# Kernel tuning notes

Measured on AMD Instinct MI355X. Metric: run time of the kernel, lower is better.

The kernel has to match this reference:

```python
import jax, jax.numpy as jnp
import numpy as np

N_GRAPHS = 512  # number of graphs in the batch
S2S_STEPS = 3   # Set2Set processing_steps


def segment_softmax(e, seg, num_seg):
    m = jax.ops.segment_max(e, seg, num_segments=num_seg)
    ex = jnp.exp(e - m[seg])
    s = jax.ops.segment_sum(ex, seg, num_segments=num_seg)
    return ex / s[seg]


def setup_inputs() -> dict:
    key = jax.random.key(0)
    ks = jax.random.split(key, 24)
    N, E, Fin, Fe, D = 30000, 480000, 25, 14, 256
    s = 0.05
    inp = {
        "x": jax.random.normal(ks[0], (N, Fin), jnp.float32),
        "edge_attr": jax.random.normal(ks[1], (E, Fe), jnp.float32),
        # lin0
        "W0": jax.random.normal(ks[2], (Fin, D), jnp.float32) * s,
        "b0": jnp.zeros((D,), jnp.float32),
        # DMPNN edge-message MLP: [x_src || e_attr] -> D -> D
        "Wm1": jax.random.normal(ks[3], (D + Fe, D), jnp.float32) * s,
        "bm1": jnp.zeros((D,), jnp.float32),
        "Wm2": jax.random.normal(ks[4], (D, D), jnp.float32) * s,
        "bm2": jnp.zeros((D,), jnp.float32),
        # node (root) update
        "Wr": jax.random.normal(ks[5], (D, D), jnp.float32) * s,
        "br": jnp.zeros((D,), jnp.float32),
        # Set2Set LSTM: input 2D -> hidden D
        "Wih": jax.random.normal(ks[6], (2 * D, 4 * D), jnp.float32) * s,
        "Whh": jax.random.normal(ks[7], (D, 4 * D), jnp.float32) * s,
        "bl": jnp.zeros((4 * D,), jnp.float32),
        # readout MLP
        "W1": jax.random.normal(ks[8], (2 * D, D), jnp.float32) * s,
        "b1": jnp.zeros((D,), jnp.float32),
        "W2": jax.random.normal(ks[9], (D, 1), jnp.float32) * s,
        "b2": jnp.zeros((1,), jnp.float32),
        "edge_index": jax.random.randint(ks[10], (2, E), 0, N, jnp.int32),
        "batch": jnp.sort(jax.random.randint(ks[11], (N,), 0, N_GRAPHS, jnp.int32)),
    }
    return inp


def reference(x, edge_attr, W0, b0, Wm1, bm1, Wm2, bm2, Wr, br,
              Wih, Whh, bl, W1, b1, W2, b2, edge_index, batch):
    N = x.shape[0]
    # lin0 + relu
    h0 = jax.nn.relu(x @ W0 + b0)  # [N, D]
    # DMPNNLayer2: edge-conditioned message, sum-aggregate, root update (eval: no dropout)
    src, dst = edge_index[0], edge_index[1]
    m = jax.nn.relu(jnp.concatenate([h0[src], edge_attr], axis=-1) @ Wm1 + bm1)  # [E, D]
    m = m @ Wm2 + bm2
    agg = jax.ops.segment_sum(m, dst, num_segments=N)  # [N, D]
    out = jax.nn.relu(h0 @ Wr + br + agg)  # relu in top-level forward, massage_depth=1
    # Set2Set pooling (processing_steps=3)
    D = out.shape[1]
    B = N_GRAPHS
    q_star = jnp.zeros((B, 2 * D), out.dtype)
    h = jnp.zeros((B, D), out.dtype)
    c = jnp.zeros((B, D), out.dtype)
    for _ in range(S2S_STEPS):
        gates = q_star @ Wih + h @ Whh + bl  # [B, 4D]
        i, f, g, o = jnp.split(gates, 4, axis=-1)
        c = jax.nn.sigmoid(f) * c + jax.nn.sigmoid(i) * jnp.tanh(g)
        h = jax.nn.sigmoid(o) * jnp.tanh(c)
        e = jnp.sum(out * h[batch], axis=-1)              # [N]
        a = segment_softmax(e, batch, B)                  # [N]
        r = jax.ops.segment_sum(a[:, None] * out, batch, num_segments=B)  # [B, D]
        q_star = jnp.concatenate([h, r], axis=-1)
    # readout (eval: dropout identity)
    y = jax.nn.relu(q_star @ W1 + b1)
    y = y @ W2 + b2
    return y.reshape(-1)
```

## Files before the change

### kernel.cpp

```cpp
#include <hip/hip_runtime.h>

typedef unsigned short u16;
typedef unsigned char u8;
typedef unsigned int u32;
using s16x8 = __attribute__((ext_vector_type(8))) short;
using s16x4 = __attribute__((ext_vector_type(4))) short;
using f32x4 = __attribute__((ext_vector_type(4))) float;

#define DEV static __device__ __forceinline__

DEV float b2f(u16 u) { return __uint_as_float(((u32)u) << 16); }
DEV u16 f2bu(float f) {
    u32 u = __float_as_uint(f);
    u32 r = (u + 0x7FFFu + ((u >> 16) & 1u)) >> 16;
    return (u16)r;
}
DEV float sigm(float x) { return 1.0f / (1.0f + expf(-x)); }

DEV float ldv(const void* p, int i, int f32flag) {
    if (f32flag) return ((const float*)p)[i];
    return b2f(((const u16*)p)[i]);
}
DEV void stv(void* p, int i, float v, int f32flag) {
    if (f32flag) ((float*)p)[i] = v;
    else ((u16*)p)[i] = f2bu(v);
}

DEV int lower_bound(const int* b, int n, int v) {
    int lo = 0, hi = n;
    while (lo < hi) { int mid = (lo + hi) >> 1; if (b[mid] < v) lo = mid + 1; else hi = mid; }
    return lo;
}

__global__ void DMPNN_Change_678604832935_kernel(int* p) {
    if (p && threadIdx.x == 0 && blockIdx.x == 0) p[0] = 1;
}

__global__ void detect_kernel(const void* x, int* flag) {
    __shared__ int cnt[128];
    int tid = threadIdx.x;
    if (tid < 128) {
        u16 v = ((const u16*)x)[tid];
        int e = (v >> 7) & 0xFF;
        cnt[tid] = (e >= 100 && e <= 141) ? 1 : 0;
    }
    __syncthreads();
    if (tid == 0) {
        int s = 0;
        for (int i = 0; i < 128; ++i) s += cnt[i];
        flag[0] = (s < 110) ? 1 : 0;
    }
}

__global__ void init_kernel(const void* x, int* flag, void* out, int* stub) {
    __shared__ int cnt[128];
    __shared__ int fsh;
    int tid = threadIdx.x;
    if (tid < 128) {
        u16 v = ((const u16*)x)[tid];
        int e = (v >> 7) & 0xFF;
        cnt[tid] = (e >= 100 && e <= 141) ? 1 : 0;
    }
    __syncthreads();
    if (tid == 0) {
        int s = 0;
        for (int i = 0; i < 128; ++i) s += cnt[i];
        int f = (s < 110) ? 1 : 0;
        flag[0] = f;
        fsh = f;
        if (stub) stub[0] = 1;
    }
    __syncthreads();
    int f32 = fsh;
    for (int i = tid; i < 512; i += 256) stv(out, i, 3.0f, f32);
}

__global__ void fillv_kernel(void* out, const int* flag, float v) {
    int i = blockIdx.x * 256 + threadIdx.x;
    if (i < 512) stv(out, i, v, flag[0]);
}

__global__ void zero_kernel(float* p, int n) {
    int i = blockIdx.x * 256 + threadIdx.x;
    int stride = gridDim.x * 256;
    for (; i < n; i += stride) p[i] = 0.0f;
}

__global__ void zero2_kernel(float* a, int na, float* b, int nb) {
    int i = blockIdx.x * 256 + threadIdx.x;
    int stride = gridDim.x * 256;
    for (int j = i; j < na; j += stride) a[j] = 0.0f;
    for (int j = i; j < nb; j += stride) b[j] = 0.0f;
}

__global__ void hist_kernel(const int* __restrict__ eidx, u32* __restrict__ cnt) {
    int i = blockIdx.x * 256 + threadIdx.x;
    if (i < 480000) atomicAdd(&cnt[eidx[480000 + i]], 1u);
}

__global__ void scan1_kernel(const u32* __restrict__ cnt, u32* __restrict__ part) {
    __shared__ u32 s[256];
    int i = blockIdx.x * 256 + threadIdx.x;
    s[threadIdx.x] = (i < 30000) ? cnt[i] : 0u;
    __syncthreads();
    for (int st = 128; st > 0; st >>= 1) {
        if (threadIdx.x < st) s[threadIdx.x] += s[threadIdx.x + st];
        __syncthreads();
    }
    if (threadIdx.x == 0) part[blockIdx.x] = s[0];
}

__global__ void scan3_kernel(u32* __restrict__ cursor, const u32* __restrict__ part) {
    __shared__ u32 s[256];
    __shared__ u32 pbase;
    int b = blockIdx.x, tid = threadIdx.x;
    {
        u32 v = (tid < 118 && tid < b) ? part[tid] : 0u;
        s[tid] = v;
        __syncthreads();
        for (int st = 128; st > 0; st >>= 1) {
            if (tid < st) s[tid] += s[tid + st];
            __syncthreads();
        }
        if (tid == 0) pbase = s[0];
        __syncthreads();
    }
    int i = b * 256 + tid;
    u32 v = (i < 30000) ? cursor[i] : 0u;
    s[tid] = v;
    __syncthreads();
    for (int off = 1; off < 256; off <<= 1) {
        u32 t = (tid >= off) ? s[tid - off] : 0u;
        __syncthreads();
        s[tid] += t;
        __syncthreads();
    }
    u32 excl = s[tid] - v + pbase;
    if (i < 30000) cursor[i] = excl;
}

__global__ void scatter_kernel(const int* __restrict__ eidx, u32* __restrict__ cursor,
                               u16* __restrict__ permLo, u8* __restrict__ permHi,
                               u16* __restrict__ srcW) {
    int i = blockIdx.x * 256 + threadIdx.x;
    if (i < 480000) {
        int d = eidx[480000 + i];
        u32 pos = atomicAdd(&cursor[d], 1u);
        permLo[pos] = (u16)(i & 0xFFFF);
        permHi[pos] = (u8)(i >> 16);
        if (srcW) srcW[pos] = (u16)eidx[i];
    }
}

__global__ void to_blocked_all(const void* Wm1, const void* Wm2, const void* Wr,
                               const void* Wih, const void* Whh,
                               const void* eattr, const int* flag,
                               u16* Wm1b, u16* Wm2b, u16* Wrb, u16* Wcatb,
                               u16* eattrB) {
    const int T1 = 9 * 4 * 256 * 8;
    const int T2 = T1 + 8 * 4 * 256 * 8;
    const int T3 = T2 + 8 * 4 * 256 * 8;
    const int T4 = T3 + 24 * 4 * 1024 * 8;
    const int T5 = T4 + 480000 * 14;
    int idx = blockIdx.x * 256 + threadIdx.x;
    int f32 = flag[0];
    if (idx >= T4) {
        if (eattrB && idx < T5) {
            int l = idx - T4;
            eattrB[l] = f2bu(ldv(eattr, l, f32));
        }
        return;
    }
    if (idx < T3) {
        const void* src; u16* dst; int K; int l;
        if (idx < T1)      { src = Wm1; dst = Wm1b; K = 270; l = idx; }
        else if (idx < T2) { src = Wm2; dst = Wm2b; K = 256; l = idx - T1; }
        else               { src = Wr;  dst = Wrb;  K = 256; l = idx - T2; }
        int c = l & 7;
        int n = (l >> 3) & 255;
        int jk = l >> 11;
        int j = jk & 3, kt = jk >> 2;
        int k = kt * 32 + j * 8 + c;
        u16 v = 0;
        if (k < K) v = f2bu(ldv(src, k * 256 + n, f32));
        dst[l] = v;
    } else {
        int l = idx - T3;
        int c = l & 7;
        int n = (l >> 3) & 1023;
        int jk = l >> 13;
        int j = jk & 3, kt = jk >> 2;
        int k = kt * 32 + j * 8 + c;
        u16 v = 0;
        if (k < 512) v = f2bu(ldv(Wih, k * 1024 + n, f32));
        else if (k < 768) v = f2bu(ldv(Whh, (k - 512) * 1024 + n, f32));
        Wcatb[l] = v;
    }
}

__global__ __launch_bounds__(256) void lin0_kernel(const void* x, const void* W0,
                                                   const void* b0, const int* flag,
                                                   u16* h0b) {
    int f32 = flag[0];
    int n0 = blockIdx.x * 8, tid = threadIdx.x;
    __shared__ float xs[8][26];
    if (tid < 200) {
        int nn = tid / 25, k = tid % 25;
        xs[nn][k] = ldv(x, (n0 + nn) * 25 + k, f32);
    }
    __syncthreads();
    float wr[25];
    #pragma unroll
    for (int k = 0; k < 25; ++k) wr[k] = ldv(W0, k * 256 + tid, f32);
    float bias = ldv(b0, tid, f32);
    #pragma unroll
    for (int nn = 0; nn < 8; ++nn) {
        float a = bias;
        #pragma unroll
        for (int k = 0; k < 25; ++k) a += xs[nn][k] * wr[k];
        h0b[(n0 + nn) * 256 + tid] = f2bu(fmaxf(a, 0.0f));
    }
}

__global__ __launch_bounds__(256) void lin0q_kernel(
    const void* x, const void* W0, const void* b0, const int* flag,
    const u16* __restrict__ Wm1b, u16* __restrict__ h0b, u16* __restrict__ Qb) {
    __shared__ __attribute__((aligned(16))) u16 As[64 * 264];
    __shared__ float xs[64][26];
    const int f32 = flag[0];
    const int tid = threadIdx.x;
    const int w = tid >> 6, lane = tid & 63, quad = lane >> 4, mrow = lane & 15;
    const int row0 = blockIdx.x * 64;
    const int colb = w * 64 + mrow;

    for (int idx = tid; idx < 64 * 25; idx += 256) {
        int i = idx / 25, k = idx - i * 25;
        int row = row0 + i;
        xs[i][k] = (row < 30000) ? ldv(x, row * 25 + k, f32) : 0.0f;
    }
    float wr[25];
    #pragma unroll
    for (int k = 0; k < 25; ++k) wr[k] = ldv(W0, k * 256 + tid, f32);
    float bias = ldv(b0, tid, f32);
    __syncthreads();
    for (int i = 0; i < 64; ++i) {
        float a = bias;
        #pragma unroll
        for (int k = 0; k < 25; ++k) a += xs[i][k] * wr[k];
        u16 hb = f2bu(fmaxf(a, 0.0f));
        As[i * 264 + tid] = hb;
        int row = row0 + i;
        if (row < 30000) h0b[row * 256 + tid] = hb;
    }
    __syncthreads();

    f32x4 acc[4][4];
    f32x4 fzero = {0.f, 0.f, 0.f, 0.f};
    #pragma unroll
    for (int mi = 0; mi < 4; ++mi)
        #pragma unroll
        for (int ni = 0; ni < 4; ++ni) acc[mi][ni] = fzero;

    for (int kt = 0; kt < 8; ++kt) {
        s16x8 af[4], bf[4];
        #pragma unroll
        for (int ni = 0; ni < 4; ++ni)
            bf[ni] = *(const s16x8*)(Wm1b + (((kt * 4 + quad) * 256) + colb + ni * 16) * 8);
        #pragma unroll
        for (int mi = 0; mi < 4; ++mi)
            af[mi] = *(const s16x8*)(As + (mi * 16 + mrow) * 264 + kt * 32 + quad * 8);
        #pragma unroll
        for (int mi = 0; mi < 4; ++mi)
            #pragma unroll
            for (int ni = 0; ni < 4; ++ni)
                acc[mi][ni] = __builtin_amdgcn_mfma_f32_16x16x32_bf16(af[mi], bf[ni], acc[mi][ni], 0, 0, 0);
    }

    #pragma unroll
    for (int mi = 0; mi < 4; ++mi)
        #pragma unroll
        for (int rg = 0; rg < 4; ++rg) {
            int row = row0 + mi * 16 + quad * 4 + rg;
            if (row >= 30000) continue;
            #pragma unroll
            for (int ni = 0; ni < 4; ++ni)
                Qb[row * 256 + colb + ni * 16] = f2bu(acc[mi][ni][rg]);
        }
}

__global__ __launch_bounds__(256) void qgen_kernel(
    const u16* __restrict__ h0b, const u16* __restrict__ Wm1b,
    u16* __restrict__ Qb) {
    __shared__ __attribute__((aligned(16))) u16 As[64 * 264];
    const int tid = threadIdx.x;
    const int w = tid >> 6, lane = tid & 63, quad = lane >> 4, mrow = lane & 15;
    const int row0 = blockIdx.x * 64;
    const int colb = w * 64 + mrow;
    const int r = tid >> 2, sub = tid & 3;

    {
        int row = row0 + r;
        u16* arow = As + r * 264;
        #pragma unroll
        for (int j = 0; j < 8; ++j) {
            int c0 = sub * 64 + j * 8;
            s16x8 v = {0, 0, 0, 0, 0, 0, 0, 0};
            if (row < 30000) v = *(const s16x8*)(h0b + row * 256 + c0);
            *(s16x8*)(arow + c0) = v;
        }
    }
    __syncthreads();

    f32x4 acc[4][4];
    f32x4 fzero = {0.f, 0.f, 0.f, 0.f};
    #pragma unroll
    for (int mi = 0; mi < 4; ++mi)
        #pragma unroll
        for (int ni = 0; ni < 4; ++ni) acc[mi][ni] = fzero;

    for (int kt = 0; kt < 8; ++kt) {
        s16x8 af[4], bf[4];
        #pragma unroll
        for (int ni = 0; ni < 4; ++ni)
            bf[ni] = *(const s16x8*)(Wm1b + (((kt * 4 + quad) * 256) + colb + ni * 16) * 8);
        #pragma unroll
        for (int mi = 0; mi < 4; ++mi)
            af[mi] = *(const s16x8*)(As + (mi * 16 + mrow) * 264 + kt * 32 + quad * 8);
        #pragma unroll
        for (int mi = 0; mi < 4; ++mi)
            #pragma unroll
            for (int ni = 0; ni < 4; ++ni)
                acc[mi][ni] = __builtin_amdgcn_mfma_f32_16x16x32_bf16(af[mi], bf[ni], acc[mi][ni], 0, 0, 0);
    }

    #pragma unroll
    for (int mi = 0; mi < 4; ++mi)
        #pragma unroll
        for (int rg = 0; rg < 4; ++rg) {
            int row = row0 + mi * 16 + quad * 4 + rg;
            if (row >= 30000) continue;
            #pragma unroll
            for (int ni = 0; ni < 4; ++ni)
                Qb[row * 256 + colb + ni * 16] = f2bu(acc[mi][ni][rg]);
        }
}

#define MAXD 96
__global__ __launch_bounds__(256) void edge_mfma_node2_kernel(
    const u16* __restrict__ Qb, const void* __restrict__ eattr,
    const u16* __restrict__ eattrB,
    const u16* __restrict__ srcW,
    const u16* __restrict__ permLo, const u8* __restrict__ permHi,
    const u32* __restrict__ cursor,
    const u16* __restrict__ Wm1b, const void* __restrict__ bm1,
    const int* __restrict__ flag, u16* __restrict__ aggB) {
    const int f32 = flag[0];
    const int n = blockIdx.x, tid = threadIdx.x;
    const int w = tid >> 6, lane = tid & 63, quad = lane >> 4, mrow = lane & 15;
    const int beg = (n > 0) ? (int)cursor[n - 1] : 0;
    const int end = (int)cursor[n];
    __shared__ int eids[MAXD];
    __shared__ int srcl[MAXD];
    __shared__ int sorted_s[MAXD];
    __shared__ int sortedSrc[MAXD];
    __shared__ __attribute__((aligned(16))) u16 Ae[16 * 40];

    const int colb = w * 64 + mrow;
    s16x8 bf[4];
    float bm1c[4];
    #pragma unroll
    for (int ni = 0; ni < 4; ++ni) {
        bf[ni] = *(const s16x8*)(Wm1b + (((32 + quad) * 256) + colb + ni * 16) * 8);
        bm1c[ni] = ldv(bm1, colb + ni * 16, f32);
    }

    float psum[4] = {0.f, 0.f, 0.f, 0.f};
    const f32x4 fzero = {0.f, 0.f, 0.f, 0.f};

    for (int base = beg; base < end; base += MAXD) {
        int wcnt = end - base; if (wcnt > MAXD) wcnt = MAXD;
        if (tid < wcnt) {
            int si = base + tid;
            eids[tid] = (int)permLo[si] | ((int)permHi[si] << 16);
            srcl[tid] = (int)srcW[si];
        }
        __syncthreads();
        if (tid < wcnt) {
            int key = eids[tid], r2 = 0;
            for (int j = 0; j < wcnt; ++j) r2 += (eids[j] < key);
            sorted_s[r2] = key;
            sortedSrc[r2] = srcl[tid];
        }
        __syncthreads();

        for (int cb = 0; cb < wcnt; cb += 16) {
            {
                int row = tid >> 4, c = tid & 15;
                int gi = cb + row;
                int e = (gi < wcnt) ? sorted_s[gi] : -1;
                u16 v = 0;
                if (e >= 0 && c < 14)
                    v = eattrB ? eattrB[e * 14 + c] : f2bu(ldv(eattr, e * 14 + c, f32));
                Ae[row * 40 + c] = v;
                Ae[row * 40 + 16 + c] = 0;
            }
            __syncthreads();

            float qv[4][4];
            #pragma unroll
            for (int rg = 0; rg < 4; ++rg) {
                int gi = cb + quad * 4 + rg;
                int sidx = (gi < wcnt) ? sortedSrc[gi] : 0;
                const u16* qrow = Qb + sidx * 256;
                #pragma unroll
                for (int ni = 0; ni < 4; ++ni)
                    qv[rg][ni] = b2f(qrow[colb + ni * 16]);
            }

            s16x8 af = *(const s16x8*)(Ae + mrow * 40 + quad * 8);
            f32x4 acc[4];
            #pragma unroll
            for (int ni = 0; ni < 4; ++ni)
                acc[ni] = __builtin_amdgcn_mfma_f32_16x16x32_bf16(af, bf[ni], fzero, 0, 0, 0);

            #pragma unroll
            for (int rg = 0; rg < 4; ++rg) {
                if (cb + quad * 4 + rg < wcnt) {
                    #pragma unroll
                    for (int ni = 0; ni < 4; ++ni)
                        psum[ni] += fmaxf(acc[ni][rg] + bm1c[ni] + qv[rg][ni], 0.0f);
                }
            }
            __syncthreads();
        }
    }

    #pragma unroll
    for (int ni = 0; ni < 4; ++ni) {
        float v = psum[ni];
        v += __shfl_xor(v, 16, 64);
        v += __shfl_xor(v, 32, 64);
        psum[ni] = v;
    }
    if (quad == 0) {
        #pragma unroll
        for (int ni = 0; ni < 4; ++ni)
            aggB[n * 256 + colb + ni * 16] = f2bu(psum[ni]);
    }
}

__global__ __launch_bounds__(256) void edge_mfma_node_kernel(
    const u16* __restrict__ Qb, const void* __restrict__ eattr,
    const int* __restrict__ eidx,
    const u16* __restrict__ permLo, const u8* __restrict__ permHi,
    const u32* __restrict__ cursor,
    const u16* __restrict__ Wm1b, const void* __restrict__ bm1,
    const int* __restrict__ flag, float* __restrict__ aggP) {
    const int f32 = flag[0];
    const int n = blockIdx.x, tid = threadIdx.x;
    const int w = tid >> 6, lane = tid & 63, quad = lane >> 4, mrow = lane & 15;
    const int beg = (n > 0) ? (int)cursor[n - 1] : 0;
    const int end = (int)cursor[n];
    __shared__ int eids[MAXD];
    __shared__ int sorted_s[MAXD];
    __shared__ int srcs16[16];
    __shared__ __attribute__((aligned(16))) u16 Ae[16 * 40];

    const int colb = w * 64 + mrow;
    s16x8 bf[4];
    float bm1c[4];
    #pragma unroll
    for (int ni = 0; ni < 4; ++ni) {
        bf[ni] = *(const s16x8*)(Wm1b + (((32 + quad) * 256) + colb + ni * 16) * 8);
        bm1c[ni] = ldv(bm1, colb + ni * 16, f32);
    }

    float psum[4] = {0.f, 0.f, 0.f, 0.f};
    const f32x4 fzero = {0.f, 0.f, 0.f, 0.f};

    for (int base = beg; base < end; base += MAXD) {
        int wcnt = end - base; if (wcnt > MAXD) wcnt = MAXD;
        if (tid < wcnt) {
            int si = base + tid;
            eids[tid] = (int)permLo[si] | ((int)permHi[si] << 16);
        }
        __syncthreads();
        if (tid < wcnt) {
            int key = eids[tid], r2 = 0;
            for (int j = 0; j < wcnt; ++j) r2 += (eids[j] < key);
            sorted_s[r2] = key;
        }
        __syncthreads();

        for (int cb = 0; cb < wcnt; cb += 16) {
            {
                int row = tid >> 4, c = tid & 15;
                int gi = cb + row;
                int e = (gi < wcnt) ? sorted_s[gi] : -1;
                u16 v = 0;
                if (e >= 0 && c < 14) v = f2bu(ldv(eattr, e * 14 + c, f32));
                Ae[row * 40 + c] = v;
                Ae[row * 40 + 16 + c] = 0;
                if (c == 0) srcs16[row] = (e >= 0) ? eidx[e] : 0;
            }
            __syncthreads();

            s16x8 af = *(const s16x8*)(Ae + mrow * 40 + quad * 8);
            f32x4 acc[4];
            #pragma unroll
            for (int ni = 0; ni < 4; ++ni)
                acc[ni] = __builtin_amdgcn_mfma_f32_16x16x32_bf16(af, bf[ni], fzero, 0, 0, 0);

            #pragma unroll
            for (int rg = 0; rg < 4; ++rg) {
                int row = quad * 4 + rg;
                if (cb + row < wcnt) {
                    const u16* qrow = Qb + srcs16[row] * 256;
                    #pragma unroll
                    for (int ni = 0; ni < 4; ++ni) {
                        float q = b2f(qrow[colb + ni * 16]);
                        psum[ni] += fmaxf(acc[ni][rg] + bm1c[ni] + q, 0.0f);
                    }
                }
            }
            __syncthreads();
        }
    }

    #pragma unroll
    for (int ni = 0; ni < 4; ++ni) {
        float v = psum[ni];
        v += __shfl_xor(v, 16, 64);
        v += __shfl_xor(v, 32, 64);
        psum[ni] = v;
    }
    if (quad == 0) {
        #pragma unroll
        for (int ni = 0; ni < 4; ++ni)
            aggP[n * 256 + colb + ni * 16] = psum[ni];
    }
}

__global__ __launch_bounds__(256) void edge_sorted_kernel(
    const u16* __restrict__ h0b, const void* __restrict__ eattr,
    const int* __restrict__ eidx,
    const u16* __restrict__ permLo, const u8* __restrict__ permHi,
    const u16* __restrict__ Wm1b,
    const void* __restrict__ bm1,
    const int* __restrict__ flag, float* __restrict__ aggP) {
    __shared__ __attribute__((aligned(16))) u16 As[64 * 296];
    __shared__ int dsh[64];
    const int f32 = flag[0];
    const int tid = threadIdx.x;
    const int w = tid >> 6, lane = tid & 63, quad = lane >> 4, mrow = lane & 15;
    const int eb0 = blockIdx.x * 64;
    const int colb = w * 64 + mrow;

    if (tid < 64) {
        int sj = eb0 + tid;
        int ee = (int)permLo[sj] | ((int)permHi[sj] << 16);
        dsh[tid] = eidx[480000 + ee];
    }
    {
        int r = tid >> 2, sub = tid & 3;
        int si = eb0 + r;
        int e = (int)permLo[si] | ((int)permHi[si] << 16);
        int src = eidx[e];
        const u16* hrow = h0b + src * 256;
        u16* arow = As + r * 296;
        #pragma unroll
        for (int j = 0; j < 8; ++j) {
            int c0 = sub * 64 + j * 8;
            *(s16x8*)(arow + c0) = *(const s16x8*)(hrow + c0);
        }
        if (sub == 0) {
            for (int c = 0; c < 14; ++c) arow[256 + c] = f2bu(ldv(eattr, e * 14 + c, f32));
            for (int c = 14; c < 40; ++c) arow[256 + c] = 0;
        }
    }
    __syncthreads();

    f32x4 acc[4][4];
    f32x4 fzero = {0.f, 0.f, 0.f, 0.f};
    #pragma unroll
    for (int mi = 0; mi < 4; ++mi)
        #pragma unroll
        for (int ni = 0; ni < 4; ++ni) acc[mi][ni] = fzero;

    for (int kt = 0; kt < 9; ++kt) {
        s16x8 af[4], bf[4];
        #pragma unroll
        for (int ni = 0; ni < 4; ++ni)
            bf[ni] = *(const s16x8*)(Wm1b + (((kt * 4 + quad) * 256) + colb + ni * 16) * 8);
        #pragma unroll
        for (int mi = 0; mi < 4; ++mi)
            af[mi] = *(const s16x8*)(As + (mi * 16 + mrow) * 296 + kt * 32 + quad * 8);
        #pragma unroll
        for (int mi = 0; mi < 4; ++mi)
            #pragma unroll
            for (int ni = 0; ni < 4; ++ni)
                acc[mi][ni] = __builtin_amdgcn_mfma_f32_16x16x32_bf16(af[mi], bf[ni], acc[mi][ni], 0, 0, 0);
    }

    float bm1c[4];
    #pragma unroll
    for (int ni = 0; ni < 4; ++ni) bm1c[ni] = ldv(bm1, colb + ni * 16, f32);
    __syncthreads();
    #pragma unroll
    for (int mi = 0; mi < 4; ++mi)
        #pragma unroll
        for (int ni = 0; ni < 4; ++ni)
            #pragma unroll
            for (int rg = 0; rg < 4; ++rg) {
                int row = mi * 16 + quad * 4 + rg;
                As[row * 296 + colb + ni * 16] = f2bu(fmaxf(acc[mi][ni][rg] + bm1c[ni], 0.0f));
            }
    __syncthreads();

    {
        int c = tid;
        float s = 0.0f;
        int cur = dsh[0];
        #pragma unroll 8
        for (int rr = 0; rr < 64; ++rr) {
            int d = dsh[rr];
            if (d != cur) { atomicAdd(&aggP[cur * 256 + c], s); s = 0.0f; cur = d; }
            s += b2f(As[rr * 296 + c]);
        }
        atomicAdd(&aggP[cur * 256 + c], s);
    }
}

__global__ __launch_bounds__(256) void node_dual_kernel(
    u16* __restrict__ h0b, const u16* __restrict__ Wrb, const u16* __restrict__ Wm2b,
    const void* __restrict__ br, const void* __restrict__ bm2,
    const void* __restrict__ aggV, int agg_bf16,
    const u32* __restrict__ cursor,
    const int* __restrict__ flag) {
    __shared__ __attribute__((aligned(16))) u16 As[64 * 264];
    const int f32 = flag[0];
    const int tid = threadIdx.x;
    const int w = tid >> 6, lane = tid & 63, quad = lane >> 4, mrow = lane & 15;
    const int row0 = blockIdx.x * 64;
    const int colb = w * 64 + mrow;
    const int r = tid >> 2, sub = tid & 3;

    {
        int row = row0 + r;
        u16* arow = As + r * 264;
        #pragma unroll
        for (int j = 0; j < 8; ++j) {
            int c0 = sub * 64 + j * 8;
            s16x8 v = {0, 0, 0, 0, 0, 0, 0, 0};
            if (row < 30000) v = *(const s16x8*)(h0b + row * 256 + c0);
            *(s16x8*)(arow + c0) = v;
        }
    }
    __syncthreads();

    f32x4 acc[4][4];
    f32x4 fzero = {0.f, 0.f, 0.f, 0.f};
    #pragma unroll
    for (int mi = 0; mi < 4; ++mi)
        #pragma unroll
        for (int ni = 0; ni < 4; ++ni) acc[mi][ni] = fzero;

    for (int kt = 0; kt < 8; ++kt) {
        s16x8 af[4], bf[4];
        #pragma unroll
        for (int ni = 0; ni < 4; ++ni)
            bf[ni] = *(const s16x8*)(Wrb + (((kt * 4 + quad) * 256) + colb + ni * 16) * 8);
        #pragma unroll
        for (int mi = 0; mi < 4; ++mi)
            af[mi] = *(const s16x8*)(As + (mi * 16 + mrow) * 264 + kt * 32 + quad * 8);
        #pragma unroll
        for (int mi = 0; mi < 4; ++mi)
            #pragma unroll
            for (int ni = 0; ni < 4; ++ni)
                acc[mi][ni] = __builtin_amdgcn_mfma_f32_16x16x32_bf16(af[mi], bf[ni], acc[mi][ni], 0, 0, 0);
    }
    __syncthreads();

    {
        int row = row0 + r;
        u16* arow = As + r * 264;
        if (agg_bf16) {
            const u16* aggB = (const u16*)aggV;
            #pragma unroll
            for (int j = 0; j < 8; ++j) {
                int c0 = sub * 64 + j * 8;
                s16x8 v = {0, 0, 0, 0, 0, 0, 0, 0};
                if (row < 30000) v = *(const s16x8*)(aggB + row * 256 + c0);
                *(s16x8*)(arow + c0) = v;
            }
        } else {
            const float* aggP = (const float*)aggV;
            #pragma unroll
            for (int j = 0; j < 8; ++j) {
                int c0 = sub * 64 + j * 8;
                s16x8 pk = {0, 0, 0, 0, 0, 0, 0, 0};
                if (row < 30000) {
                    f32x4 a = *(const f32x4*)(aggP + row * 256 + c0);
                    f32x4 b = *(const f32x4*)(aggP + row * 256 + c0 + 4);
                    pk[0] = (short)f2bu(a[0]); pk[1] = (short)f2bu(a[1]);
                    pk[2] = (short)f2bu(a[2]); pk[3] = (short)f2bu(a[3]);
                    pk[4] = (short)f2bu(b[0]); pk[5] = (short)f2bu(b[1]);
                    pk[6] = (short)f2bu(b[2]); pk[7] = (short)f2bu(b[3]);
                }
                *(s16x8*)(arow + c0) = pk;
            }
        }
    }
    __syncthreads();

    for (int kt = 0; kt < 8; ++kt) {
        s16x8 af[4], bf[4];
        #pragma unroll
        for (int ni = 0; ni < 4; ++ni)
            bf[ni] = *(const s16x8*)(Wm2b + (((kt * 4 + quad) * 256) + colb + ni * 16) * 8);
        #pragma unroll
        for (int mi = 0; mi < 4; ++mi)
            af[mi] = *(const s16x8*)(As + (mi * 16 + mrow) * 264 + kt * 32 + quad * 8);
        #pragma unroll
        for (int mi = 0; mi < 4; ++mi)
            #pragma unroll
            for (int ni = 0; ni < 4; ++ni)
                acc[mi][ni] = __builtin_amdgcn_mfma_f32_16x16x32_bf16(af[mi], bf[ni], acc[mi][ni], 0, 0, 0);
    }

    #pragma unroll
    for (int mi = 0; mi < 4; ++mi)
        #pragma unroll
        for (int rg = 0; rg < 4; ++rg) {
            int row = row0 + mi * 16 + quad * 4 + rg;
            if (row >= 30000) continue;
            float dg = (float)(cursor[row] - (row > 0 ? cursor[row - 1] : 0u));
            #pragma unroll
            for (int ni = 0; ni < 4; ++ni) {
                int col = colb + ni * 16;
                float v = acc[mi][ni][rg] + ldv(br, col, f32) + dg * ldv(bm2, col, f32);
                h0b[row * 256 + col] = f2bu(fmaxf(v, 0.0f));
            }
        }
}

__global__ __launch_bounds__(256) void gates_mfma_kernel(
    const u16* __restrict__ Abuf, const u16* __restrict__ Wcatb,
    float* __restrict__ G) {
    const int tid = threadIdx.x;
    const int w = tid >> 6, lane = tid & 63, quad = lane >> 4, mrow = lane & 15;
    const int row0 = blockIdx.x * 64;
    const int col = blockIdx.y * 64 + w * 16 + mrow;

    f32x4 acc[4];
    f32x4 fzero = {0.f, 0.f, 0.f, 0.f};
    #pragma unroll
    for (int mi = 0; mi < 4; ++mi) acc[mi] = fzero;

    for (int kt = 0; kt < 24; ++kt) {
        s16x8 bfv = *(const s16x8*)(Wcatb + (((kt * 4 + quad) * 1024) + col) * 8);
        s16x8 af[4];
        #pragma unroll
        for (int mi = 0; mi < 4; ++mi)
            af[mi] = *(const s16x8*)(Abuf + (row0 + mi * 16 + mrow) * 768 + kt * 32 + quad * 8);
        #pragma unroll
        for (int mi = 0; mi < 4; ++mi)
            acc[mi] = __builtin_amdgcn_mfma_f32_16x16x32_bf16(af[mi], bfv, acc[mi], 0, 0, 0);
    }

    #pragma unroll
    for (int mi = 0; mi < 4; ++mi)
        #pragma unroll
        for (int rg = 0; rg < 4; ++rg)
            G[(row0 + mi * 16 + quad * 4 + rg) * 1024 + col] = acc[mi][rg];
}

#define GROWS 112
__global__ __launch_bounds__(256) void s2s_lstm_fused_kernel(
    const float* __restrict__ G, const void* __restrict__ bl,
    const int* __restrict__ flag, float* __restrict__ Cst, float* __restrict__ Hst,
    const u16* __restrict__ outb, const int* __restrict__ batch,
    float* __restrict__ Rst, u16* __restrict__ Abuf, float* __restrict__ ebuf) {
    __shared__ __attribute__((aligned(16))) u16 Ls[GROWS * 256];
    __shared__ __attribute__((aligned(16))) float hsh[256];
    __shared__ float esh[GROWS];
    __shared__ float red[256];
    const int b = blockIdx.x, tid = threadIdx.x;
    const int w = tid >> 6, lane = tid & 63;
    const int f32 = flag[0];

    {
        float gi = G[b * 1024 + tid]       + ldv(bl, tid, f32);
        float gf = G[b * 1024 + 256 + tid] + ldv(bl, 256 + tid, f32);
        float gg = G[b * 1024 + 512 + tid] + ldv(bl, 512 + tid, f32);
        float go = G[b * 1024 + 768 + tid] + ldv(bl, 768 + tid, f32);
        float c = Cst[b * 256 + tid];
        c = sigm(gf) * c + sigm(gi) * tanhf(gg);
        Cst[b * 256 + tid] = c;
        float h = sigm(go) * tanhf(c);
        Hst[b * 256 + tid] = h;
        u16 hb = f2bu(h);
        Abuf[b * 768 + tid] = hb;
        Abuf[b * 768 + 512 + tid] = hb;
        hsh[tid] = h;
    }
    const int n0 = lower_bound(batch, 30000, b);
    const int n1 = lower_bound(batch, 30000, b + 1);
    const int cnt = n1 - n0;
    __syncthreads();
    float r_out = 0.0f;
    if (cnt > 0 && cnt <= GROWS) {
        for (int idx = tid; idx < cnt * 32; idx += 256) {
            int i = idx >> 5, c8 = idx & 31;
            *(s16x8*)(Ls + i * 256 + c8 * 8) = *(const s16x8*)(outb + (n0 + i) * 256 + c8 * 8);
        }
        __syncthreads();
        for (int i = w; i < cnt; i += 4) {
            s16x4 ov = *(const s16x4*)(Ls + i * 256 + lane * 4);
            f32x4 hv = *(const f32x4*)(hsh + lane * 4);
            float p = b2f((u16)ov[0]) * hv[0] + b2f((u16)ov[1]) * hv[1]
                    + b2f((u16)ov[2]) * hv[2] + b2f((u16)ov[3]) * hv[3];
            #pragma unroll
            for (int off = 1; off < 64; off <<= 1) p += __shfl_xor(p, off, 64);
            if (lane == 0) esh[i] = p;
        }
        __syncthreads();
        float m = -1e30f;
        for (int i = tid; i < cnt; i += 256) m = fmaxf(m, esh[i]);
        red[tid] = m; __syncthreads();
        for (int s = 128; s > 0; s >>= 1) { if (tid < s) red[tid] = fmaxf(red[tid], red[tid + s]); __syncthreads(); }
        m = red[0]; __syncthreads();
        float sl = 0.0f;
        for (int i = tid; i < cnt; i += 256) { float pe = expf(esh[i] - m); esh[i] = pe; sl += pe; }
        red[tid] = sl; __syncthreads();
        for (int s = 128; s > 0; s >>= 1) { if (tid < s) red[tid] += red[tid + s]; __syncthreads(); }
        float ssum = red[0]; __syncthreads();
        float acc = 0.0f;
        for (int i = 0; i < cnt; ++i) acc += esh[i] * b2f(Ls[i * 256 + tid]);
        r_out = acc / ssum;
    } else if (cnt > GROWS) {
        for (int i = w; i < cnt; i += 4) {
            const u16* orow = outb + (n0 + i) * 256 + lane * 4;
            f32x4 hv = *(const f32x4*)(hsh + lane * 4);
            float p = b2f(orow[0]) * hv[0] + b2f(orow[1]) * hv[1]
                    + b2f(orow[2]) * hv[2] + b2f(orow[3]) * hv[3];
            #pragma unroll
            for (int off = 1; off < 64; off <<= 1) p += __shfl_xor(p, off, 64);
            if (lane == 0) ebuf[n0 + i] = p;
        }
        __syncthreads();
        float m = -1e30f;
        for (int n = n0 + tid; n < n1; n += 256) m = fmaxf(m, ebuf[n]);
        red[tid] = m; __syncthreads();
        for (int s = 128; s > 0; s >>= 1) { if (tid < s) red[tid] = fmaxf(red[tid], red[tid + s]); __syncthreads(); }
        m = red[0]; __syncthreads();
        float sl = 0.0f;
        for (int n = n0 + tid; n < n1; n += 256) sl += expf(ebuf[n] - m);
        red[tid] = sl; __syncthreads();
        for (int s = 128; s > 0; s >>= 1) { if (tid < s) red[tid] += red[tid + s]; __syncthreads(); }
        float ssum = red[0]; __syncthreads();
        float acc = 0.0f;
        for (int c0 = n0; c0 < n1; c0 += 256) {
            int nn = n1 - c0; if (nn > 256) nn = 256;
            __syncthreads();
            if (tid < nn) red[tid] = expf(ebuf[c0 + tid] - m);
            __syncthreads();
            for (int i = 0; i < nn; ++i) acc += red[i] * b2f(outb[(c0 + i) * 256 + tid]);
        }
        r_out = acc / ssum;
    }
    Rst[b * 256 + tid] = r_out;
    Abuf[b * 768 + 256 + tid] = f2bu(r_out);
}

__global__ __launch_bounds__(256) void readout_kernel(const float* Hst, const float* Rst,
                                                      const void* W1, const void* b1,
                                                      const void* W2, const void* b2,
                                                      const u16* nodeout, const void* aggV,
                                                      int agg_bf16,
                                                      const int* flag, void* out) {
    int f32 = flag[0];
    int b = blockIdx.x, tid = threadIdx.x;
    __shared__ float qs[512];
    __shared__ float red[256];
    qs[tid] = Hst[b * 256 + tid];
    qs[256 + tid] = Rst[b * 256 + tid];
    __syncthreads();
    float a = ldv(b1, tid, f32);
    if (f32) {
        const float* W1f = (const float*)W1;
        #pragma unroll 8
        for (int k = 0; k < 512; ++k) a += qs[k] * W1f[k * 256 + tid];
    } else {
        const u16* W1h = (const u16*)W1;
        #pragma unroll 8
        for (int k = 0; k < 512; ++k) a += qs[k] * b2f(W1h[k * 256 + tid]);
    }
    a = fmaxf(a, 0.0f) * ldv(W2, tid, f32);
    red[tid] = a; __syncthreads();
    for (int s = 128; s > 0; s >>= 1) { if (tid < s) red[tid] += red[tid + s]; __syncthreads(); }
    if (tid == 0) {
        float D = 0.0f;
        if (b == 0) {
            float s1 = 0.0f, s2 = 0.0f, s3 = 0.0f;
            for (int i = 0; i < 256; ++i) {
                s1 += fabsf(b2f(nodeout[i]));
                s2 += agg_bf16 ? fabsf(b2f(((const u16*)aggV)[i]))
                               : fabsf(((const float*)aggV)[i]);
                s3 += fabsf(Rst[i]);
            }
            if (s1 < 1e-3f) D += 100.0f;
            if (s2 < 1e-3f) D += 200.0f;
            if (s3 < 1e-6f) D += 400.0f;
        }
        stv(out, b, red[0] + ldv(b2, 0, f32) + D, f32);
    }
}

#define OFF_FLAG 0
#define OFF_HST  64
#define OFF_RST  524352
#define OFF_CST  1048640
#define OFF_PLO  64
#define OFF_PHI  960064
#define OFF_CUR  1440064
#define OFF_WREG 1572928
#define OFF_WM1B (OFF_WREG)
#define OFF_WM2B (OFF_WREG + 147456)
#define OFF_WRB  (OFF_WREG + 278528)
#define OFF_WCAT (OFF_WREG + 409600)
#define OFF_E    3670080
#define OFF_AGG  3790144
#define OFF_ABUF (OFF_AGG + 1048576)
#define OFF_G    (OFF_AGG + 4194304)
#define OFF_H0B  34510144
#define WS_NEEDED 49870144
#define OFF_Q    49870144
#define WS_FAST  (49870144 + 15360000)
#define OFF_SRC  (OFF_Q + 15360000)
#define WS_FAST2 (OFF_SRC + 960000)
#define OFF_EATB (OFF_SRC + 960000)
#define WS_FAST3 (OFF_EATB + 13440000)

extern "C" __attribute__((visibility("default")))
void kernel_launch(void* const* d_in, const int* in_sizes, int n_in,
                   void* d_out, int out_size, void* d_ws, size_t ws_size,
                   hipStream_t stream) {
    char* ws = (char*)d_ws;
    int*   flag   = (int*)(ws + OFF_FLAG);
    float* Hst    = (float*)(ws + OFF_HST);
    float* Rst    = (float*)(ws + OFF_RST);
    float* Cst    = (float*)(ws + OFF_CST);
    u16*   permLo = (u16*)(ws + OFF_PLO);
    u8*    permHi = (u8*)(ws + OFF_PHI);
    u32*   cursor = (u32*)(ws + OFF_CUR);
    u16*   Wm1b   = (u16*)(ws + OFF_WM1B);
    u16*   Wm2b   = (u16*)(ws + OFF_WM2B);
    u16*   Wrb    = (u16*)(ws + OFF_WRB);
    u16*   Wcatb  = (u16*)(ws + OFF_WCAT);
    float* ebuf   = (float*)(ws + OFF_E);
    u32*   part   = (u32*)(ws + OFF_E);
    float* aggP   = (float*)(ws + OFF_AGG);
    u16*   Abuf   = (u16*)(ws + OFF_ABUF);
    float* G      = (float*)(ws + OFF_G);
    u16*   h0b    = (u16*)(ws + OFF_H0B);
    u16*   Qb     = (u16*)(ws + OFF_Q);
    u16*   srcW   = (u16*)(ws + OFF_SRC);
    u16*   eattrB = (u16*)(ws + OFF_EATB);

    bool sizes_ok = (n_in == 19)
        && in_sizes[0] == 30000 * 25
        && in_sizes[1] == 480000 * 14
        && in_sizes[4] == 270 * 256
        && in_sizes[10] == 512 * 1024
        && in_sizes[17] == 2 * 480000
        && in_sizes[18] == 30000;
    if (!sizes_ok) {
        detect_kernel<<<1, 256, 0, stream>>>(d_in[0], flag);
        fillv_kernel<<<2, 256, 0, stream>>>(d_out, flag, 1600.0f);
        return;
    }
    if (ws_size < (size_t)WS_NEEDED) {
        detect_kernel<<<1, 256, 0, stream>>>(d_in[0], flag);
        fillv_kernel<<<2, 256, 0, stream>>>(d_out, flag, 800.0f);
        return;
    }
    const int fastlvl = (ws_size >= (size_t)WS_FAST3) ? 3
                      : (ws_size >= (size_t)WS_FAST2) ? 2
                      : (ws_size >= (size_t)WS_FAST)  ? 1 : 0;

    const void* x     = d_in[0];
    const void* eattr = d_in[1];
    const void* W0    = d_in[2];
    const void* b0    = d_in[3];
    const void* Wm1   = d_in[4];
    const void* bm1   = d_in[5];
    const void* Wm2   = d_in[6];
    const void* bm2   = d_in[7];
    const void* Wr    = d_in[8];
    const void* br    = d_in[9];
    const void* Wih   = d_in[10];
    const void* Whh   = d_in[11];
    const void* bl    = d_in[12];
    const void* W1    = d_in[13];
    const void* b1    = d_in[14];
    const void* W2    = d_in[15];
    const void* b2    = d_in[16];
    const int* eidx   = (const int*)d_in[17];
    const int* batch  = (const int*)d_in[18];

    init_kernel<<<1, 256, 0, stream>>>(x, flag, d_out, (int*)(ws + OFF_G));

    {
        int total = (fastlvl >= 3) ? (991232 + 480000 * 14) : 991232;
        int grid = (total + 255) / 256;
        to_blocked_all<<<grid, 256, 0, stream>>>(Wm1, Wm2, Wr, Wih, Whh, eattr, flag,
                                                 Wm1b, Wm2b, Wrb, Wcatb,
                                                 (fastlvl >= 3) ? eattrB : (u16*)nullptr);
    }

    if (fastlvl >= 1) {
        lin0q_kernel<<<469, 256, 0, stream>>>(x, W0, b0, flag, Wm1b, h0b, Qb);
    } else {
        lin0_kernel<<<3750, 256, 0, stream>>>(x, W0, b0, flag, h0b);
    }

    zero_kernel<<<30, 256, 0, stream>>>((float*)cursor, 30000);
    hist_kernel<<<1875, 256, 0, stream>>>(eidx, cursor);
    scan1_kernel<<<118, 256, 0, stream>>>(cursor, part);
    scan3_kernel<<<118, 256, 0, stream>>>(cursor, part);
    scatter_kernel<<<1875, 256, 0, stream>>>(eidx, cursor, permLo, permHi,
                                             (fastlvl >= 2) ? srcW : (u16*)nullptr);

    int agg_bf16 = 0;
    if (fastlvl >= 2) {
        agg_bf16 = 1;
        edge_mfma_node2_kernel<<<30000, 256, 0, stream>>>(
            Qb, eattr, (fastlvl >= 3) ? eattrB : (u16*)nullptr,
            srcW, permLo, permHi, cursor, Wm1b, bm1, flag, (u16*)aggP);
    } else if (fastlvl == 1) {
        edge_mfma_node_kernel<<<30000, 256, 0, stream>>>(Qb, eattr, eidx, permLo, permHi,
                                                         cursor, Wm1b, bm1, flag, aggP);
    } else {
        zero_kernel<<<1024, 256, 0, stream>>>(aggP, 7680000);
        edge_sorted_kernel<<<7500, 256, 0, stream>>>(h0b, eattr, eidx, permLo, permHi,
                                                     Wm1b, bm1, flag, aggP);
    }
    node_dual_kernel<<<469, 256, 0, stream>>>(h0b, Wrb, Wm2b, br, bm2,
                                              aggP, agg_bf16, cursor, flag);

    zero2_kernel<<<256, 256, 0, stream>>>(Cst, 131072, (float*)Abuf, 196608);

    for (int s = 0; s < 3; ++s) {
        gates_mfma_kernel<<<dim3(8, 16), 256, 0, stream>>>(Abuf, Wcatb, G);
        s2s_lstm_fused_kernel<<<512, 256, 0, stream>>>(G, bl, flag, Cst, Hst,
                                                       h0b, batch, Rst, Abuf, ebuf);
    }
    readout_kernel<<<512, 256, 0, stream>>>(Hst, Rst, W1, b1, W2, b2, h0b,
                                            aggP, agg_bf16, flag, d_out);
}
```

Baseline: 460.0 us.

## Pre-permute edge attributes by destination and add simplified per-node edge kernel

During the scatter pass, the bf16 edge attributes are copied into destination-sorted order in a new workspace buffer. A new per-node edge kernel then reads those attributes contiguously together with the sorted source indices, with no permutation lookups and no per-node sorting or staging of edge ids. This is meant to cut gather indirection and shared-memory bookkeeping in the edge stage. In exchange it needs extra workspace and a scattered 14-element copy per edge in the scatter kernel, and it only runs when the workspace is large enough.

```diff
diff --git a/kernel.cpp b/kernel.cpp
--- a/kernel.cpp
+++ b/kernel.cpp
@@ -141,7 +141,8 @@
 
 __global__ void scatter_kernel(const int* __restrict__ eidx, u32* __restrict__ cursor,
                                u16* __restrict__ permLo, u8* __restrict__ permHi,
-                               u16* __restrict__ srcW) {
+                               u16* __restrict__ srcW,
+                               const u16* __restrict__ eattrB, u16* __restrict__ eattrS) {
     int i = blockIdx.x * 256 + threadIdx.x;
     if (i < 480000) {
         int d = eidx[480000 + i];
@@ -149,6 +150,10 @@
         permLo[pos] = (u16)(i & 0xFFFF);
         permHi[pos] = (u8)(i >> 16);
         if (srcW) srcW[pos] = (u16)eidx[i];
+        if (eattrS) {
+            #pragma unroll
+            for (int c = 0; c < 14; ++c) eattrS[pos * 14 + c] = eattrB[i * 14 + c];
+        }
     }
 }
 
@@ -346,6 +351,85 @@
 }
 
 #define MAXD 96
+__global__ __launch_bounds__(256) void edge_mfma_node3_kernel(
+    const u16* __restrict__ Qb, const u16* __restrict__ eattrS,
+    const u16* __restrict__ srcW,
+    const u32* __restrict__ cursor,
+    const u16* __restrict__ Wm1b, const void* __restrict__ bm1,
+    const int* __restrict__ flag, u16* __restrict__ aggB) {
+    const int f32 = flag[0];
+    const int n = blockIdx.x, tid = threadIdx.x;
+    const int w = tid >> 6, lane = tid & 63, quad = lane >> 4, mrow = lane & 15;
+    const int beg = (n > 0) ? (int)cursor[n - 1] : 0;
+    const int end = (int)cursor[n];
+    __shared__ int srcs16[16];
+    __shared__ __attribute__((aligned(16))) u16 Ae[16 * 40];
+
+    const int colb = w * 64 + mrow;
+    s16x8 bf[4];
+    float bm1c[4];
+    #pragma unroll
+    for (int ni = 0; ni < 4; ++ni) {
+        bf[ni] = *(const s16x8*)(Wm1b + (((32 + quad) * 256) + colb + ni * 16) * 8);
+        bm1c[ni] = ldv(bm1, colb + ni * 16, f32);
+    }
+
+    float psum[4] = {0.f, 0.f, 0.f, 0.f};
+    const f32x4 fzero = {0.f, 0.f, 0.f, 0.f};
+
+    for (int cb = beg; cb < end; cb += 16) {
+        int m = end - cb; if (m > 16) m = 16;
+        {
+            int row = tid >> 4, c = tid & 15;
+            u16 v = 0;
+            if (row < m && c < 14) v = eattrS[(cb + row) * 14 + c];
+            Ae[row * 40 + c] = v;
+            Ae[row * 40 + 16 + c] = 0;
+            if (c == 0) srcs16[row] = (row < m) ? (int)srcW[cb + row] : 0;
+        }
+        __syncthreads();
+
+        float qv[4][4];
+        #pragma unroll
+        for (int rg = 0; rg < 4; ++rg) {
+            int sidx = srcs16[quad * 4 + rg];
+            const u16* qrow = Qb + sidx * 256;
+            #pragma unroll
+            for (int ni = 0; ni < 4; ++ni)
+                qv[rg][ni] = b2f(qrow[colb + ni * 16]);
+        }
+
+        s16x8 af = *(const s16x8*)(Ae + mrow * 40 + quad * 8);
+        f32x4 acc[4];
+        #pragma unroll
+        for (int ni = 0; ni < 4; ++ni)
+            acc[ni] = __builtin_amdgcn_mfma_f32_16x16x32_bf16(af, bf[ni], fzero, 0, 0, 0);
+
+        #pragma unroll
+        for (int rg = 0; rg < 4; ++rg) {
+            if (quad * 4 + rg < m) {
+                #pragma unroll
+                for (int ni = 0; ni < 4; ++ni)
+                    psum[ni] += fmaxf(acc[ni][rg] + bm1c[ni] + qv[rg][ni], 0.0f);
+            }
+        }
+        __syncthreads();
+    }
+
+    #pragma unroll
+    for (int ni = 0; ni < 4; ++ni) {
+        float v = psum[ni];
+        v += __shfl_xor(v, 16, 64);
+        v += __shfl_xor(v, 32, 64);
+        psum[ni] = v;
+    }
+    if (quad == 0) {
+        #pragma unroll
+        for (int ni = 0; ni < 4; ++ni)
+            aggB[n * 256 + colb + ni * 16] = f2bu(psum[ni]);
+    }
+}
+
 __global__ __launch_bounds__(256) void edge_mfma_node2_kernel(
     const u16* __restrict__ Qb, const void* __restrict__ eattr,
     const u16* __restrict__ eattrB,
@@ -941,6 +1025,8 @@
 #define WS_FAST2 (OFF_SRC + 960000)
 #define OFF_EATB (OFF_SRC + 960000)
 #define WS_FAST3 (OFF_EATB + 13440000)
+#define OFF_EATS (OFF_EATB + 13440000)
+#define WS_FAST4 (OFF_EATS + 13440000)
 
 extern "C" __attribute__((visibility("default")))
 void kernel_launch(void* const* d_in, const int* in_sizes, int n_in,
@@ -967,6 +1053,7 @@
     u16*   Qb     = (u16*)(ws + OFF_Q);
     u16*   srcW   = (u16*)(ws + OFF_SRC);
     u16*   eattrB = (u16*)(ws + OFF_EATB);
+    u16*   eattrS = (u16*)(ws + OFF_EATS);
 
     bool sizes_ok = (n_in == 19)
         && in_sizes[0] == 30000 * 25
@@ -985,7 +1072,8 @@
         fillv_kernel<<<2, 256, 0, stream>>>(d_out, flag, 800.0f);
         return;
     }
-    const int fastlvl = (ws_size >= (size_t)WS_FAST3) ? 3
+    const int fastlvl = (ws_size >= (size_t)WS_FAST4) ? 4
+                      : (ws_size >= (size_t)WS_FAST3) ? 3
                       : (ws_size >= (size_t)WS_FAST2) ? 2
                       : (ws_size >= (size_t)WS_FAST)  ? 1 : 0;
 
@@ -1030,10 +1118,16 @@
     scan1_kernel<<<118, 256, 0, stream>>>(cursor, part);
     scan3_kernel<<<118, 256, 0, stream>>>(cursor, part);
     scatter_kernel<<<1875, 256, 0, stream>>>(eidx, cursor, permLo, permHi,
-                                             (fastlvl >= 2) ? srcW : (u16*)nullptr);
+                                             (fastlvl >= 2) ? srcW : (u16*)nullptr,
+                                             eattrB,
+                                             (fastlvl >= 4) ? eattrS : (u16*)nullptr);
 
     int agg_bf16 = 0;
-    if (fastlvl >= 2) {
+    if (fastlvl >= 4) {
+        agg_bf16 = 1;
+        edge_mfma_node3_kernel<<<30000, 256, 0, stream>>>(
+            Qb, eattrS, srcW, cursor, Wm1b, bm1, flag, (u16*)aggP);
+    } else if (fastlvl >= 2) {
         agg_bf16 = 1;
         edge_mfma_node2_kernel<<<30000, 256, 0, stream>>>(
             Qb, eattr, (fastlvl >= 3) ? eattrB : (u16*)nullptr,
```

Result: slower. 478.3 us (+4.0%).
